# Kernel optimization log

Hardware: AMD Instinct MI355X
Metric: run time of the kernel (lower is better)

Reference implementation:

```python
import jax, jax.numpy as jnp
import numpy as np

B, D = 8192, 256


def setup_inputs() -> dict:
    key = jax.random.key(0)
    k1, k2 = jax.random.split(key)
    pred = jax.random.normal(k1, (B, D), dtype=jnp.float32)
    target = jax.random.normal(k2, (B, D), dtype=jnp.float32)
    noise_sigma = jnp.asarray(1.0, dtype=jnp.float32)  # learned scalar parameter
    return {"pred": pred, "target": target, "noise_sigma": noise_sigma}


def reference(pred, target, noise_sigma):
    # noise_var = sigma^2; MVN(pred_i, noise_var*I).log_prob(target_j)
    #   = -0.5*||target_j - pred_i||^2 / noise_var - 0.5*d*log(2*pi*noise_var)
    noise_var = noise_sigma ** 2
    d = pred.shape[-1]
    n = pred.shape[0]
    # pairwise squared distances via matmul (no [B,B,d] materialization)
    p2 = jnp.sum(pred * pred, axis=-1)      # [B]
    t2 = jnp.sum(target * target, axis=-1)  # [B]
    cross = pred @ target.T                 # [B, B]
    sqdist = p2[:, None] + t2[None, :] - 2.0 * cross  # [B, B]
    log_norm = 0.5 * d * jnp.log(2.0 * jnp.pi * noise_var)
    logits = -0.5 * sqdist / noise_var - log_norm  # [B, B]
    # cross_entropy(logits, arange(B)): mean over rows of -log_softmax diag
    logp = jax.nn.log_softmax(logits, axis=1)
    loss = -jnp.mean(jnp.diagonal(logp))
    # loss scaled by detached 2*noise_var
    return loss * jax.lax.stop_gradient(2.0 * noise_var)
```

## Files before the change

### kernel.cpp

```cpp
#include <hip/hip_runtime.h>
#include <stdint.h>

#define BATCH 8192
#define DIM 256
#define NSPLIT 16
#define BM 256
#define BN 32
#define COLS_PER_SPLIT (BATCH / NSPLIT)
#define NTILES (COLS_PER_SPLIT / BN)
#define LOG2E 1.4426950408889634f
#define LN2   0.6931471805599453f

typedef unsigned short ushort_t;
typedef __bf16 bf16x8 __attribute__((ext_vector_type(8)));
typedef float floatx4 __attribute__((ext_vector_type(4)));
typedef float floatx2 __attribute__((ext_vector_type(2)));

__device__ __forceinline__ float fast_exp2(float x) {
#if __has_builtin(__builtin_amdgcn_exp2f)
    return __builtin_amdgcn_exp2f(x);
#else
    return exp2f(x);
#endif
}

__device__ __forceinline__ ushort_t f2bf(float f) {
    uint32_t u = __float_as_uint(f);
    u += 0x7fffu + ((u >> 16) & 1u);
    return (ushort_t)(u >> 16);
}

__global__ __launch_bounds__(256) void prep_kernel(
        const float* __restrict__ pred, const float* __restrict__ target,
        ushort_t* __restrict__ Ap, ushort_t* __restrict__ Bp,
        float* __restrict__ t2, float* __restrict__ diag) {
    __shared__ __align__(16) ushort_t ldsA[4096];
    __shared__ __align__(16) ushort_t ldsB[4096];
    const int t = threadIdx.x;
    const int r = t >> 4, c = t & 15;
    const int rt = blockIdx.x;
    const int row = rt * 16 + r;

    float dsum = 0.f, tsum = 0.f;
#pragma unroll
    for (int q = 0; q < 4; ++q) {
        const int k0 = q * 64 + c * 4;
        const float4 p4 = *(const float4*)(pred + (size_t)row * DIM + k0);
        const float4 t4 = *(const float4*)(target + (size_t)row * DIM + k0);
        dsum += p4.x * t4.x + p4.y * t4.y + p4.z * t4.z + p4.w * t4.w;
        tsum += t4.x * t4.x + t4.y * t4.y + t4.z * t4.z + t4.w * t4.w;
        const int kc = 2 * q + (c >> 3);
        const int kg = (c >> 1) & 3;
        const int e  = (c & 1) * 4;
        const int off = kc * 512 + kg * 128 + r * 8 + e;
        ushort4 pv, tv;
        pv.x = f2bf(p4.x); pv.y = f2bf(p4.y); pv.z = f2bf(p4.z); pv.w = f2bf(p4.w);
        tv.x = f2bf(t4.x); tv.y = f2bf(t4.y); tv.z = f2bf(t4.z); tv.w = f2bf(t4.w);
        *(ushort4*)(ldsA + off) = pv;
        *(ushort4*)(ldsB + off) = tv;
    }
#pragma unroll
    for (int mask = 1; mask < 16; mask <<= 1) {
        dsum += __shfl_xor(dsum, mask);
        tsum += __shfl_xor(tsum, mask);
    }
    if (c == 0) { diag[row] = dsum; t2[row] = tsum; }
    __syncthreads();

    const size_t abase = (size_t)rt * 4096;
    const size_t bbase = (size_t)(rt >> 2) * 16384 + (size_t)(rt & 3) * 512;
#pragma unroll
    for (int i = 0; i < 2; ++i) {
        const int g = i * 256 + t;
        const uint4 va = *(const uint4*)(ldsA + g * 8);
        const uint4 vb = *(const uint4*)(ldsB + g * 8);
        *(uint4*)(Ap + abase + (size_t)g * 8) = va;
        *(uint4*)(Bp + bbase + (size_t)(g >> 6) * 2048 + (size_t)(g & 63) * 8) = vb;
    }
}

__global__ __launch_bounds__(256, 2) void main_kernel(
        const ushort_t* __restrict__ Ap, const ushort_t* __restrict__ Bp,
        const float* __restrict__ t2, const float* __restrict__ sigma,
        float2* __restrict__ partials) {
    __shared__ __align__(16) ushort_t ldsB[2][BN * DIM];

    const int lane   = threadIdx.x & 63;
    const int wave   = threadIdx.x >> 6;
    const int rowBlk = blockIdx.x;
    const int split  = blockIdx.y;

    const float sg = sigma[0];
    const float inv_nv = 1.0f / (sg * sg);
    const float c1 = LOG2E * inv_nv;
    const float c2 = -0.5f * c1;
    const float floor2 = -108.0f * c1;

    bf16x8 afrag[4][8];
#pragma unroll
    for (int mt = 0; mt < 4; ++mt) {
        const ushort_t* base = Ap + (size_t)(rowBlk * 16 + wave * 4 + mt) * 4096 + lane * 8;
#pragma unroll
        for (int kc = 0; kc < 8; ++kc)
            afrag[mt][kc] = *(const bf16x8*)(base + kc * 512);
    }

    floatx2 m2[4][2], l2[4][2];
#pragma unroll
    for (int mt = 0; mt < 4; ++mt)
#pragma unroll
        for (int rp = 0; rp < 2; ++rp) {
            m2[mt][rp] = (floatx2){floor2, floor2};
            l2[mt][rp] = (floatx2){0.f, 0.f};
        }

    {
        const int j0 = split * COLS_PER_SPLIT;
        const size_t jt = (size_t)(j0 >> 6);
        const int hb = (j0 >> 5) & 1;
        const char* gbase = (const char*)(Bp + jt * 16384 + (size_t)hb * 1024);
#pragma unroll
        for (int q = 0; q < 4; ++q) {
            const int c = wave * 4 + q;
            const size_t goff = (size_t)(c >> 1) * 4096 + (size_t)(c & 1) * 1024;
            __builtin_amdgcn_global_load_lds(
                (const __attribute__((address_space(1))) void*)(gbase + goff + (size_t)lane * 16),
                (__attribute__((address_space(3))) void*)((char*)ldsB[0] + c * 1024),
                16, 0, 0);
        }
    }
    __syncthreads();

    for (int ct = 0; ct < NTILES; ++ct) {
        const ushort_t* cur = ldsB[ct & 1];
        const int j0 = split * COLS_PER_SPLIT + ct * BN;

        if (ct + 1 < NTILES) {
            const int j1 = j0 + BN;
            const size_t jt = (size_t)(j1 >> 6);
            const int hb = (j1 >> 5) & 1;
            const char* gbase = (const char*)(Bp + jt * 16384 + (size_t)hb * 1024);
            char* lbase = (char*)ldsB[(ct + 1) & 1];
#pragma unroll
            for (int q = 0; q < 4; ++q) {
                const int c = wave * 4 + q;
                const size_t goff = (size_t)(c >> 1) * 4096 + (size_t)(c & 1) * 1024;
                __builtin_amdgcn_global_load_lds(
                    (const __attribute__((address_space(1))) void*)(gbase + goff + (size_t)lane * 16),
                    (__attribute__((address_space(3))) void*)(lbase + c * 1024),
                    16, 0, 0);
            }
        }

        float t2v0 = t2[j0 + (lane & 15)];
        float t2v1 = t2[j0 + 16 + (lane & 15)];

        floatx4 acc[4][2];
#pragma unroll
        for (int mt = 0; mt < 4; ++mt)
#pragma unroll
            for (int nt = 0; nt < 2; ++nt)
                acc[mt][nt] = (floatx4){0.f, 0.f, 0.f, 0.f};

#pragma unroll
        for (int kc = 0; kc < 8; ++kc) {
            const bf16x8 b0 = *(const bf16x8*)(cur + (kc * 2 + 0) * 512 + lane * 8);
            const bf16x8 b1 = *(const bf16x8*)(cur + (kc * 2 + 1) * 512 + lane * 8);
#pragma unroll
            for (int mt = 0; mt < 4; ++mt) {
                acc[mt][0] = __builtin_amdgcn_mfma_f32_16x16x32_bf16(afrag[mt][kc], b0, acc[mt][0], 0, 0, 0);
                acc[mt][1] = __builtin_amdgcn_mfma_f32_16x16x32_bf16(afrag[mt][kc], b1, acc[mt][1], 0, 0, 0);
            }
        }

        const float tvc0 = t2v0 * c2;
        const float tvc1 = t2v1 * c2;

        if (ct == 0) {
#pragma unroll
            for (int mt = 0; mt < 4; ++mt)
#pragma unroll
                for (int rp = 0; rp < 2; ++rp) {
                    const floatx2 v0 = (floatx2){acc[mt][0][2 * rp], acc[mt][0][2 * rp + 1]} * c1 + tvc0;
                    const floatx2 v1 = (floatx2){acc[mt][1][2 * rp], acc[mt][1][2 * rp + 1]} * c1 + tvc1;
                    floatx2 mm = __builtin_elementwise_max(v0, v1);
                    mm = __builtin_elementwise_max(mm, (floatx2){floor2, floor2});
                    m2[mt][rp] = mm;
                    floatx2 s;
                    s.x = fast_exp2(v0.x - mm.x) + fast_exp2(v1.x - mm.x);
                    s.y = fast_exp2(v0.y - mm.y) + fast_exp2(v1.y - mm.y);
                    l2[mt][rp] = s;
                }
        } else {
#pragma unroll
            for (int mt = 0; mt < 4; ++mt)
#pragma unroll
                for (int rp = 0; rp < 2; ++rp) {
                    const floatx2 mm = m2[mt][rp];
                    const floatx2 v0 = (floatx2){acc[mt][0][2 * rp], acc[mt][0][2 * rp + 1]} * c1 + (tvc0 - mm);
                    const floatx2 v1 = (floatx2){acc[mt][1][2 * rp], acc[mt][1][2 * rp + 1]} * c1 + (tvc1 - mm);
                    floatx2 s = l2[mt][rp];
                    s.x += fast_exp2(v0.x) + fast_exp2(v1.x);
                    s.y += fast_exp2(v0.y) + fast_exp2(v1.y);
                    l2[mt][rp] = s;
                }
        }

        __syncthreads();
    }

#pragma unroll
    for (int mt = 0; mt < 4; ++mt)
#pragma unroll
        for (int rp = 0; rp < 2; ++rp)
#pragma unroll
            for (int z = 0; z < 2; ++z) {
                float m = m2[mt][rp][z];
                float l = l2[mt][rp][z];
#pragma unroll
                for (int mask = 1; mask < 16; mask <<= 1) {
                    const float mo = __shfl_xor(m, mask);
                    const float lo = __shfl_xor(l, mask);
                    const float mn = fmaxf(m, mo);
                    l = l * fast_exp2(m - mn) + lo * fast_exp2(mo - mn);
                    m = mn;
                }
                if ((lane & 15) == 0) {
                    const int r  = rp * 2 + z;
                    const int rw = rowBlk * BM + wave * 64 + mt * 16 + (lane >> 4) * 4 + r;
                    partials[(size_t)split * BATCH + rw] = make_float2(m, l);
                }
            }
}

__global__ __launch_bounds__(256) void finish1_kernel(
        const float2* __restrict__ partials, const float* __restrict__ t2,
        const float* __restrict__ diag, const float* __restrict__ sigma,
        float* __restrict__ bsum) {
    __shared__ float red[256];
    const int tid = threadIdx.x;
    const int row = blockIdx.x * 256 + tid;
    const float sg = sigma[0];
    const float inv_nv = 1.0f / (sg * sg);

    float2 p[NSPLIT];
    float m = -__builtin_inff();
#pragma unroll
    for (int s = 0; s < NSPLIT; ++s) {
        p[s] = partials[(size_t)s * BATCH + row];
        m = fmaxf(m, p[s].x);
    }
    float L = 0.0f;
#pragma unroll
    for (int s = 0; s < NSPLIT; ++s)
        L += p[s].y * fast_exp2(p[s].x - m);
    const float lse_nat = LN2 * (m + __log2f(L));
    const float d = (diag[row] - 0.5f * t2[row]) * inv_nv;
    red[tid] = lse_nat - d;
    __syncthreads();
    for (int s = 128; s > 0; s >>= 1) {
        if (tid < s) red[tid] += red[tid + s];
        __syncthreads();
    }
    if (tid == 0) bsum[blockIdx.x] = red[0];
}

__global__ __launch_bounds__(64) void finish2_kernel(
        const float* __restrict__ bsum, const float* __restrict__ sigma,
        float* __restrict__ out) {
    const int tid = threadIdx.x;
    float v = (tid < 32) ? bsum[tid] : 0.0f;
#pragma unroll
    for (int mask = 32; mask > 0; mask >>= 1)
        v += __shfl_xor(v, mask);
    if (tid == 0) {
        const float nv = sigma[0] * sigma[0];
        out[0] = 2.0f * nv * v / (float)BATCH;
    }
}

extern "C" void kernel_launch(void* const* d_in, const int* in_sizes, int n_in,
                              void* d_out, int out_size, void* d_ws, size_t ws_size,
                              hipStream_t stream) {
    const float* pred   = (const float*)d_in[0];
    const float* target = (const float*)d_in[1];
    const float* sigma  = (const float*)d_in[2];
    float* out = (float*)d_out;

    char* ws = (char*)d_ws;
    ushort_t* Ap  = (ushort_t*)(ws);
    ushort_t* Bp  = (ushort_t*)(ws + (size_t)BATCH * DIM * 2);
    float* t2     = (float*)(ws + (size_t)BATCH * DIM * 4);
    float* diag   = (float*)(ws + (size_t)BATCH * DIM * 4 + BATCH * 4);
    float2* parts = (float2*)(ws + (size_t)BATCH * DIM * 4 + (size_t)BATCH * 8);
    float* bsum   = (float*)(ws + (size_t)BATCH * DIM * 4 + (size_t)BATCH * 8
                             + (size_t)NSPLIT * BATCH * 8);

    prep_kernel<<<BATCH / 16, 256, 0, stream>>>(pred, target, Ap, Bp, t2, diag);
    main_kernel<<<dim3(BATCH / BM, NSPLIT), 256, 0, stream>>>(Ap, Bp, t2, sigma, parts);
    finish1_kernel<<<BATCH / 256, 256, 0, stream>>>(parts, t2, diag, sigma, bsum);
    finish2_kernel<<<1, 64, 0, stream>>>(bsum, sigma, out);
}
```

Measured before the change: 105.2 us.

## Switch cross-product GEMM from bf16 to fp8 scaled MFMA

Prep now quantizes pred and target to fp8 e4m3 and writes them in a new packed layout matching the 16x16x128 f8f6f4 MFMA operand format. The main kernel loads fp8 A fragments and B tiles, halving staged bytes, and issues a quarter as many MFMAs with unit scales. This cuts matrix-core work and memory traffic, but fp8 rounding on large-magnitude logits risks accuracy loss in the softmax loss.

```diff
diff --git a/kernel.cpp b/kernel.cpp
--- a/kernel.cpp
+++ b/kernel.cpp
@@ -12,9 +12,10 @@
 #define LN2   0.6931471805599453f
 
 typedef unsigned short ushort_t;
-typedef __bf16 bf16x8 __attribute__((ext_vector_type(8)));
 typedef float floatx4 __attribute__((ext_vector_type(4)));
 typedef float floatx2 __attribute__((ext_vector_type(2)));
+typedef int intx4 __attribute__((ext_vector_type(4)));
+typedef int intx8 __attribute__((ext_vector_type(8)));
 
 __device__ __forceinline__ float fast_exp2(float x) {
 #if __has_builtin(__builtin_amdgcn_exp2f)
@@ -24,18 +25,12 @@
 #endif
 }
 
-__device__ __forceinline__ ushort_t f2bf(float f) {
-    uint32_t u = __float_as_uint(f);
-    u += 0x7fffu + ((u >> 16) & 1u);
-    return (ushort_t)(u >> 16);
-}
-
 __global__ __launch_bounds__(256) void prep_kernel(
         const float* __restrict__ pred, const float* __restrict__ target,
-        ushort_t* __restrict__ Ap, ushort_t* __restrict__ Bp,
+        uint8_t* __restrict__ Ap, uint8_t* __restrict__ Bp,
         float* __restrict__ t2, float* __restrict__ diag) {
-    __shared__ __align__(16) ushort_t ldsA[4096];
-    __shared__ __align__(16) ushort_t ldsB[4096];
+    __shared__ __align__(16) uint8_t ldsA[4096];
+    __shared__ __align__(16) uint8_t ldsB[4096];
     const int t = threadIdx.x;
     const int r = t >> 4, c = t & 15;
     const int rt = blockIdx.x;
@@ -49,15 +44,17 @@
         const float4 t4 = *(const float4*)(target + (size_t)row * DIM + k0);
         dsum += p4.x * t4.x + p4.y * t4.y + p4.z * t4.z + p4.w * t4.w;
         tsum += t4.x * t4.x + t4.y * t4.y + t4.z * t4.z + t4.w * t4.w;
-        const int kc = 2 * q + (c >> 3);
-        const int kg = (c >> 1) & 3;
-        const int e  = (c & 1) * 4;
-        const int off = kc * 512 + kg * 128 + r * 8 + e;
-        ushort4 pv, tv;
-        pv.x = f2bf(p4.x); pv.y = f2bf(p4.y); pv.z = f2bf(p4.z); pv.w = f2bf(p4.w);
-        tv.x = f2bf(t4.x); tv.y = f2bf(t4.y); tv.z = f2bf(t4.z); tv.w = f2bf(t4.w);
-        *(ushort4*)(ldsA + off) = pv;
-        *(ushort4*)(ldsB + off) = tv;
+        const int kstep  = k0 >> 7;
+        const int kgroup = (k0 >> 5) & 3;
+        const int half   = (k0 >> 4) & 1;
+        const int b      = k0 & 15;
+        const int off = kstep * 2048 + half * 1024 + (kgroup * 16 + r) * 16 + b;
+        int pp = __builtin_amdgcn_cvt_pk_fp8_f32(p4.x, p4.y, 0, false);
+        pp     = __builtin_amdgcn_cvt_pk_fp8_f32(p4.z, p4.w, pp, true);
+        int tt = __builtin_amdgcn_cvt_pk_fp8_f32(t4.x, t4.y, 0, false);
+        tt     = __builtin_amdgcn_cvt_pk_fp8_f32(t4.z, t4.w, tt, true);
+        *(int*)(ldsA + off) = pp;
+        *(int*)(ldsB + off) = tt;
     }
 #pragma unroll
     for (int mask = 1; mask < 16; mask <<= 1) {
@@ -67,23 +64,18 @@
     if (c == 0) { diag[row] = dsum; t2[row] = tsum; }
     __syncthreads();
 
-    const size_t abase = (size_t)rt * 4096;
-    const size_t bbase = (size_t)(rt >> 2) * 16384 + (size_t)(rt & 3) * 512;
-#pragma unroll
-    for (int i = 0; i < 2; ++i) {
-        const int g = i * 256 + t;
-        const uint4 va = *(const uint4*)(ldsA + g * 8);
-        const uint4 vb = *(const uint4*)(ldsB + g * 8);
-        *(uint4*)(Ap + abase + (size_t)g * 8) = va;
-        *(uint4*)(Bp + bbase + (size_t)(g >> 6) * 2048 + (size_t)(g & 63) * 8) = vb;
-    }
+    const size_t base = (size_t)rt * 4096;
+    const uint4 va = *(const uint4*)(ldsA + t * 16);
+    const uint4 vb = *(const uint4*)(ldsB + t * 16);
+    *(uint4*)(Ap + base + (size_t)t * 16) = va;
+    *(uint4*)(Bp + base + (size_t)t * 16) = vb;
 }
 
 __global__ __launch_bounds__(256, 2) void main_kernel(
-        const ushort_t* __restrict__ Ap, const ushort_t* __restrict__ Bp,
+        const uint8_t* __restrict__ Ap, const uint8_t* __restrict__ Bp,
         const float* __restrict__ t2, const float* __restrict__ sigma,
         float2* __restrict__ partials) {
-    __shared__ __align__(16) ushort_t ldsB[2][BN * DIM];
+    __shared__ __align__(16) uint8_t ldsB[2][BN * DIM];
 
     const int lane   = threadIdx.x & 63;
     const int wave   = threadIdx.x >> 6;
@@ -96,13 +88,16 @@
     const float c2 = -0.5f * c1;
     const float floor2 = -108.0f * c1;
 
-    bf16x8 afrag[4][8];
+    intx8 afrag[4][2];
 #pragma unroll
     for (int mt = 0; mt < 4; ++mt) {
-        const ushort_t* base = Ap + (size_t)(rowBlk * 16 + wave * 4 + mt) * 4096 + lane * 8;
-#pragma unroll
-        for (int kc = 0; kc < 8; ++kc)
-            afrag[mt][kc] = *(const bf16x8*)(base + kc * 512);
+        const uint8_t* base = Ap + (size_t)(rowBlk * 16 + wave * 4 + mt) * 4096 + lane * 16;
+#pragma unroll
+        for (int ks = 0; ks < 2; ++ks) {
+            const intx4 lo = *(const intx4*)(base + ks * 2048);
+            const intx4 hi = *(const intx4*)(base + ks * 2048 + 1024);
+            afrag[mt][ks] = (intx8){lo.x, lo.y, lo.z, lo.w, hi.x, hi.y, hi.z, hi.w};
+        }
     }
 
     floatx2 m2[4][2], l2[4][2];
@@ -116,38 +111,31 @@
 
     {
         const int j0 = split * COLS_PER_SPLIT;
-        const size_t jt = (size_t)(j0 >> 6);
-        const int hb = (j0 >> 5) & 1;
-        const char* gbase = (const char*)(Bp + jt * 16384 + (size_t)hb * 1024);
-#pragma unroll
-        for (int q = 0; q < 4; ++q) {
-            const int c = wave * 4 + q;
-            const size_t goff = (size_t)(c >> 1) * 4096 + (size_t)(c & 1) * 1024;
+        const char* gbase = (const char*)(Bp + (size_t)(j0 >> 4) * 4096);
+#pragma unroll
+        for (int q = 0; q < 2; ++q) {
+            const int ch = wave * 2 + q;
             __builtin_amdgcn_global_load_lds(
-                (const __attribute__((address_space(1))) void*)(gbase + goff + (size_t)lane * 16),
-                (__attribute__((address_space(3))) void*)((char*)ldsB[0] + c * 1024),
+                (const __attribute__((address_space(1))) void*)(gbase + ch * 1024 + (size_t)lane * 16),
+                (__attribute__((address_space(3))) void*)((char*)ldsB[0] + ch * 1024),
                 16, 0, 0);
         }
     }
     __syncthreads();
 
     for (int ct = 0; ct < NTILES; ++ct) {
-        const ushort_t* cur = ldsB[ct & 1];
+        const uint8_t* cur = ldsB[ct & 1];
         const int j0 = split * COLS_PER_SPLIT + ct * BN;
 
         if (ct + 1 < NTILES) {
-            const int j1 = j0 + BN;
-            const size_t jt = (size_t)(j1 >> 6);
-            const int hb = (j1 >> 5) & 1;
-            const char* gbase = (const char*)(Bp + jt * 16384 + (size_t)hb * 1024);
+            const char* gbase = (const char*)(Bp + (size_t)((j0 + BN) >> 4) * 4096);
             char* lbase = (char*)ldsB[(ct + 1) & 1];
 #pragma unroll
-            for (int q = 0; q < 4; ++q) {
-                const int c = wave * 4 + q;
-                const size_t goff = (size_t)(c >> 1) * 4096 + (size_t)(c & 1) * 1024;
+            for (int q = 0; q < 2; ++q) {
+                const int ch = wave * 2 + q;
                 __builtin_amdgcn_global_load_lds(
-                    (const __attribute__((address_space(1))) void*)(gbase + goff + (size_t)lane * 16),
-                    (__attribute__((address_space(3))) void*)(lbase + c * 1024),
+                    (const __attribute__((address_space(1))) void*)(gbase + ch * 1024 + (size_t)lane * 16),
+                    (__attribute__((address_space(3))) void*)(lbase + ch * 1024),
                     16, 0, 0);
             }
         }
@@ -163,13 +151,21 @@
                 acc[mt][nt] = (floatx4){0.f, 0.f, 0.f, 0.f};
 
 #pragma unroll
-        for (int kc = 0; kc < 8; ++kc) {
-            const bf16x8 b0 = *(const bf16x8*)(cur + (kc * 2 + 0) * 512 + lane * 8);
-            const bf16x8 b1 = *(const bf16x8*)(cur + (kc * 2 + 1) * 512 + lane * 8);
-#pragma unroll
-            for (int mt = 0; mt < 4; ++mt) {
-                acc[mt][0] = __builtin_amdgcn_mfma_f32_16x16x32_bf16(afrag[mt][kc], b0, acc[mt][0], 0, 0, 0);
-                acc[mt][1] = __builtin_amdgcn_mfma_f32_16x16x32_bf16(afrag[mt][kc], b1, acc[mt][1], 0, 0, 0);
+        for (int ks = 0; ks < 2; ++ks) {
+#pragma unroll
+            for (int nt = 0; nt < 2; ++nt) {
+                const uint8_t* bb = cur + nt * 4096 + ks * 2048 + lane * 16;
+                const intx4 lo = *(const intx4*)(bb);
+                const intx4 hi = *(const intx4*)(bb + 1024);
+                const intx8 bfrag = (intx8){lo.x, lo.y, lo.z, lo.w, hi.x, hi.y, hi.z, hi.w};
+#pragma unroll
+                for (int mt = 0; mt < 4; ++mt) {
+                    acc[mt][nt] = __builtin_amdgcn_mfma_scale_f32_16x16x128_f8f6f4(
+                        afrag[mt][ks], bfrag, acc[mt][nt],
+                        0, 0,
+                        0, 127,
+                        0, 127);
+                }
             }
         }
 
@@ -288,8 +284,8 @@
     float* out = (float*)d_out;
 
     char* ws = (char*)d_ws;
-    ushort_t* Ap  = (ushort_t*)(ws);
-    ushort_t* Bp  = (ushort_t*)(ws + (size_t)BATCH * DIM * 2);
+    uint8_t* Ap   = (uint8_t*)(ws);
+    uint8_t* Bp   = (uint8_t*)(ws + (size_t)BATCH * DIM);
     float* t2     = (float*)(ws + (size_t)BATCH * DIM * 4);
     float* diag   = (float*)(ws + (size_t)BATCH * DIM * 4 + BATCH * 4);
     float2* parts = (float2*)(ws + (size_t)BATCH * DIM * 4 + (size_t)BATCH * 8);
```

New measurement: 96.25 us. 8.5% less time.
